# Kernel optimization log

Hardware: AMD Instinct MI355X
Metric: run time of the kernel (lower is better)

## Reference

```python
import jax, jax.numpy as jnp
import numpy as np
import math

EMBED_DIM = 1024
N_HEADS = 16
HEAD_DIM = EMBED_DIM // N_HEADS
B, N = 2, 2048


def setup_inputs() -> dict:
    key = jax.random.key(0)
    k1, k2, k3 = jax.random.split(key, 3)
    x = jax.random.normal(k1, (B, N, EMBED_DIM), dtype=jnp.float32)
    # Per-head Linear(D, 3*head_dim), stacked over heads. PyTorch Linear init scale ~1/sqrt(fan_in).
    bound = 1.0 / math.sqrt(EMBED_DIM)
    Wkqv = jax.random.uniform(k2, (N_HEADS, EMBED_DIM, 3 * HEAD_DIM), dtype=jnp.float32, minval=-bound, maxval=bound)
    bkqv = jax.random.uniform(k3, (N_HEADS, 3 * HEAD_DIM), dtype=jnp.float32, minval=-bound, maxval=bound)
    return {"x": x, "Wkqv": Wkqv, "bkqv": bkqv}


def reference(x, Wkqv, bkqv):
    Bx, Nx, D = x.shape
    hd = Wkqv.shape[-1] // 3
    # all heads at once: [B, H, N, 3*hd]
    proj = jnp.einsum('bnd,hdf->bhnf', x, Wkqv) + bkqv[None, :, None, :]
    # torch.split order in the original is (k, q, v)
    k, q, v = jnp.split(proj, 3, axis=-1)
    # scores = q @ k^T / sqrt(head_dim)   [B, H, N, N]
    scores = jnp.einsum('bhqd,bhkd->bhqk', q, k) / math.sqrt(hd)
    causal = jnp.tril(jnp.ones((Nx, Nx), dtype=bool))
    scores = jnp.where(causal[None, None, :, :], scores, -jnp.inf)
    attn = jax.nn.softmax(scores, axis=-1)
    out = jnp.einsum('bhqk,bhkd->bhqd', attn, v)  # [B, H, N, hd]
    # concat heads -> [B, N, D]  (forward() passes no out_matrix, so no output projection)
    return out.transpose(0, 2, 1, 3).reshape(Bx, Nx, D)
```

## Files before the change

### kernel.cpp

```cpp
#include <hip/hip_runtime.h>
#include <math.h>

typedef float f32x4 __attribute__((ext_vector_type(4)));
typedef __bf16 bf16x8 __attribute__((ext_vector_type(8)));
typedef __bf16 bf16x4 __attribute__((ext_vector_type(4)));

#define MFMA16(a, b, c) __builtin_amdgcn_mfma_f32_16x16x32_bf16((a), (b), (c), 0, 0, 0)

constexpr int Bsz = 2, Nseq = 2048, Dm = 1024, Hh = 16, HDim = 64, F3 = 192;
constexpr int Mrows = Bsz * Nseq;
constexpr int NC = Hh * F3;
constexpr float QSCALE = 0.125f * 1.4426950408889634f;

__device__ inline void load_lds16(const void* g, void* l) {
    __builtin_amdgcn_global_load_lds((const __attribute__((address_space(1))) void*)g,
                                     (__attribute__((address_space(3))) void*)l, 16, 0, 0);
}

#define FENCE asm volatile("" ::: "memory")
#define BARRIER do { FENCE; __builtin_amdgcn_s_barrier(); FENCE; } while (0)


__global__ __launch_bounds__(256) void conv_x_kernel(const float* __restrict__ x,
                                                     __bf16* __restrict__ xb) {
    int i = blockIdx.x * 256 + threadIdx.x;
    const float4* xv = reinterpret_cast<const float4*>(x);
    float4 a = xv[2 * i];
    float4 b = xv[2 * i + 1];
    bf16x8 o = {(__bf16)a.x, (__bf16)a.y, (__bf16)a.z, (__bf16)a.w,
                (__bf16)b.x, (__bf16)b.y, (__bf16)b.z, (__bf16)b.w};
    *reinterpret_cast<bf16x8*>(xb + 8 * i) = o;
}

__global__ __launch_bounds__(256) void conv_w_kernel(const float* __restrict__ w,
                                                     __bf16* __restrict__ wt) {
    __shared__ __bf16 tile[32][66];
    int h = blockIdx.z, d0 = blockIdx.x * 32, c0 = blockIdx.y * 64;
    for (int i = threadIdx.x; i < 32 * 64; i += 256) {
        int di = i >> 6, cj = i & 63;
        tile[di][cj] = (__bf16)w[(size_t)(h * Dm + d0 + di) * F3 + c0 + cj];
    }
    __syncthreads();
    for (int i = threadIdx.x; i < 32 * 64; i += 256) {
        int ci = i >> 5, dj = i & 31;
        wt[(size_t)(h * F3 + c0 + ci) * Dm + d0 + dj] = tile[dj][ci];
    }
}

__global__ __launch_bounds__(512, 2) void gemm_proj(const __bf16* __restrict__ xb,
                                                    const __bf16* __restrict__ wt,
                                                    const float* __restrict__ bias,
                                                    __bf16* __restrict__ kbuf,
                                                    __bf16* __restrict__ qbuf,
                                                    __bf16* __restrict__ vt) {
    __shared__ __align__(16) __bf16 Ab[2][256 * 64];
    __shared__ __align__(16) __bf16 Bb[2][192 * 64];

    int flat = blockIdx.x;
    int swz = (flat & 7) * 32 + (flat >> 3);
    int bm = swz >> 4, bn = swz & 15;
    int r0 = bm * 256, n0 = bn * 192;

    int w = threadIdx.x >> 6, lane = threadIdx.x & 63;
    int col = lane & 15, quad = lane >> 4;
    int wm = w >> 2, wn = w & 3;

    f32x4 acc[8][3] = {};

    int rl = lane >> 3;
    int cg = ((lane & 7) ^ rl) * 8;

    auto stage = [&](int t, int s) {
#pragma unroll
        for (int i = 0; i < 4; i++) {
            int rowb = w * 32 + i * 8;
            load_lds16(xb + (size_t)(r0 + rowb + rl) * Dm + t * 64 + cg,
                       &Ab[s][rowb * 64]);
        }
#pragma unroll
        for (int i = 0; i < 3; i++) {
            int rowb = w * 24 + i * 8;
            load_lds16(wt + (size_t)(n0 + rowb + rl) * Dm + t * 64 + cg,
                       &Bb[s][rowb * 64]);
        }
    };

    stage(0, 0);
    stage(1, 1);

    for (int j = 0; j < 16; j++) {
        int s = j & 1;
        if (j < 15) asm volatile("s_waitcnt vmcnt(7)" ::: "memory");
        else        asm volatile("s_waitcnt vmcnt(0)" ::: "memory");
        BARRIER;

#pragma unroll
        for (int ks = 0; ks < 2; ks++) {
            int cq = ks * 4 + quad;
            bf16x8 af[8], bfr[3];
#pragma unroll
            for (int mt = 0; mt < 8; mt++) {
                int row = wm * 128 + mt * 16 + col;
                af[mt] = *reinterpret_cast<const bf16x8*>(
                    &Ab[s][row * 64 + ((cq ^ (row & 7)) * 8)]);
            }
#pragma unroll
            for (int nt = 0; nt < 3; nt++) {
                int row = wn * 48 + nt * 16 + col;
                bfr[nt] = *reinterpret_cast<const bf16x8*>(
                    &Bb[s][row * 64 + ((cq ^ (row & 7)) * 8)]);
            }
            __builtin_amdgcn_s_setprio(1);
#pragma unroll
            for (int mt = 0; mt < 8; mt++)
#pragma unroll
                for (int nt = 0; nt < 3; nt++)
                    acc[mt][nt] = MFMA16(af[mt], bfr[nt], acc[mt][nt]);
            __builtin_amdgcn_s_setprio(0);
        }

        BARRIER;
        if (j + 2 < 16) stage(j + 2, s);
    }

#pragma unroll
    for (int nt = 0; nt < 3; nt++) {
        int g = n0 + wn * 48 + nt * 16 + col;
        int h = g / F3, c = g - h * F3;
        float bv = bias[g];
        bool isq = (c >= 64 && c < 128), isv = (c >= 128);
        int cd = c & 63;
#pragma unroll
        for (int mt = 0; mt < 8; mt++) {
#pragma unroll
            for (int rg = 0; rg < 4; rg++) {
                int r = r0 + wm * 128 + mt * 16 + quad * 4 + rg;
                int b = r >> 11, n = r & (Nseq - 1);
                float v = acc[mt][nt][rg] + bv;
                if (isq) v *= QSCALE;
                size_t bh = (size_t)(b * Hh + h);
                if (isv) {
                    int np = (n & ~63) | ((n & 15) << 2) | ((n >> 4) & 3);
                    vt[(bh * HDim + cd) * Nseq + np] = (__bf16)v;
                } else {
                    ((isq) ? qbuf : kbuf)[(bh * Nseq + n) * HDim + cd] = (__bf16)v;
                }
            }
        }
    }
}

__global__ __launch_bounds__(256) void proj_small(const float* __restrict__ x,
                                                  const __bf16* __restrict__ wt,
                                                  const float* __restrict__ bias,
                                                  __bf16* __restrict__ kbuf,
                                                  __bf16* __restrict__ qbuf,
                                                  __bf16* __restrict__ vt) {
    int h = blockIdx.y;
    int wave = threadIdx.x >> 6, lane = threadIdx.x & 63;
    int col = lane & 15, quad = lane >> 4;
    int r0 = blockIdx.x * 128 + wave * 32;

    f32x4 acc[12][2] = {};
    const float* xr0 = x + (size_t)(r0 + col) * Dm + quad * 8;
    const float* xr1 = xr0 + 16 * Dm;
    const __bf16* wbase = wt + (size_t)(h * F3 + col) * Dm + quad * 8;

    for (int k0 = 0; k0 < Dm; k0 += 32) {
        float4 a0lo = *reinterpret_cast<const float4*>(xr0 + k0);
        float4 a0hi = *reinterpret_cast<const float4*>(xr0 + k0 + 4);
        float4 a1lo = *reinterpret_cast<const float4*>(xr1 + k0);
        float4 a1hi = *reinterpret_cast<const float4*>(xr1 + k0 + 4);
        bf16x8 a0 = {(__bf16)a0lo.x, (__bf16)a0lo.y, (__bf16)a0lo.z, (__bf16)a0lo.w,
                     (__bf16)a0hi.x, (__bf16)a0hi.y, (__bf16)a0hi.z, (__bf16)a0hi.w};
        bf16x8 a1 = {(__bf16)a1lo.x, (__bf16)a1lo.y, (__bf16)a1lo.z, (__bf16)a1lo.w,
                     (__bf16)a1hi.x, (__bf16)a1hi.y, (__bf16)a1hi.z, (__bf16)a1hi.w};
#pragma unroll
        for (int ct = 0; ct < 12; ct++) {
            bf16x8 bf = *reinterpret_cast<const bf16x8*>(wbase + ct * 16 * Dm + k0);
            acc[ct][0] = MFMA16(a0, bf, acc[ct][0]);
            acc[ct][1] = MFMA16(a1, bf, acc[ct][1]);
        }
    }
#pragma unroll
    for (int ct = 0; ct < 12; ct++) {
        int c = ct * 16 + col;
        float bv = bias[h * F3 + c];
        int cd = c & 63;
        bool isq = (c >= 64 && c < 128), isv = (c >= 128);
#pragma unroll
        for (int rt = 0; rt < 2; rt++) {
#pragma unroll
            for (int rg = 0; rg < 4; rg++) {
                int r = r0 + rt * 16 + quad * 4 + rg;
                int b = r >> 11, n = r & (Nseq - 1);
                float v = acc[ct][rt][rg] + bv;
                if (isq) v *= QSCALE;
                size_t bh = (size_t)(b * Hh + h);
                if (isv) {
                    int np = (n & ~63) | ((n & 15) << 2) | ((n >> 4) & 3);
                    vt[(bh * HDim + cd) * Nseq + np] = (__bf16)v;
                } else {
                    ((isq) ? qbuf : kbuf)[(bh * Nseq + n) * HDim + cd] = (__bf16)v;
                }
            }
        }
    }
}

__global__ __launch_bounds__(256) void attn_kernel(const __bf16* __restrict__ qbuf,
                                                   const __bf16* __restrict__ kbuf,
                                                   const __bf16* __restrict__ vt,
                                                   float* __restrict__ out) {
    __shared__ __align__(16) __bf16 Kb[2][64 * 64];
    __shared__ __align__(16) __bf16 Vb[2][64 * 64];
    __shared__ __align__(16) __bf16 plds[4][16][72];
    int bh = blockIdx.x;
    int b = bh >> 4, h = bh & 15;
    int tile = 31 - blockIdx.y;
    int wave = threadIdx.x >> 6, lane = threadIdx.x & 63;
    int col = lane & 15, quad = lane >> 4;
    int q0 = tile * 64 + wave * 16;

    const __bf16* qbase = qbuf + (size_t)bh * Nseq * HDim;
    const __bf16* kbase = kbuf + (size_t)bh * Nseq * HDim;
    const __bf16* vbase = vt + (size_t)bh * HDim * Nseq;

    bf16x8 aq0 = *reinterpret_cast<const bf16x8*>(qbase + (q0 + col) * HDim + quad * 8);
    bf16x8 aq1 = *reinterpret_cast<const bf16x8*>(qbase + (q0 + col) * HDim + quad * 8 + 32);

    const bf16x8 vone = {(__bf16)1.f, (__bf16)1.f, (__bf16)1.f, (__bf16)1.f,
                         (__bf16)1.f, (__bf16)1.f, (__bf16)1.f, (__bf16)1.f};

    f32x4 o[4] = {};
    f32x4 ls = {};

    int mb = tile * 64;
    int loop_end = mb + 64;

    int rl = lane >> 3;
    int srow0 = wave * 16 + rl;
    int srow1 = wave * 16 + 8 + rl;
    int sc = (lane & 7) ^ rl;
    const __bf16* ksrc0 = kbase + srow0 * HDim + sc * 8;
    const __bf16* ksrc1 = kbase + srow1 * HDim + sc * 8;
    const __bf16* vsrc0 = vbase + (size_t)srow0 * Nseq + sc * 8;
    const __bf16* vsrc1 = vbase + (size_t)srow1 * Nseq + sc * 8;
    int d0 = wave * 1024, d1 = wave * 1024 + 512;

    int sw0 = ((quad ^ (col & 7)) * 8);
    int sw1 = (((quad + 4) ^ (col & 7)) * 8);

    load_lds16(ksrc0, &Kb[0][d0]);
    load_lds16(ksrc1, &Kb[0][d1]);
    load_lds16(vsrc0, &Vb[0][d0]);
    load_lds16(vsrc1, &Vb[0][d1]);
    FENCE;

    int s = 0;
    for (int kb = 0; kb < loop_end; kb += 64) {
        asm volatile("s_waitcnt vmcnt(0)" ::: "memory");
        BARRIER;
        int nkb = kb + 64;
        if (nkb < loop_end) {
            load_lds16(ksrc0 + nkb * HDim, &Kb[s ^ 1][d0]);
            load_lds16(ksrc1 + nkb * HDim, &Kb[s ^ 1][d1]);
            load_lds16(vsrc0 + nkb, &Vb[s ^ 1][d0]);
            load_lds16(vsrc1 + nkb, &Vb[s ^ 1][d1]);
        }

        bool masked = (kb == mb);
        const __bf16* Kcur = Kb[s];
        const __bf16* Vcur = Vb[s];
        f32x4 z = {};
        f32x4 sc4[4];
#pragma unroll
        for (int g = 0; g < 4; g++) {
            const __bf16* krow = Kcur + (col + 16 * g) * 64;
            bf16x8 k0 = *reinterpret_cast<const bf16x8*>(krow + sw0);
            bf16x8 k1 = *reinterpret_cast<const bf16x8*>(krow + sw1);
            sc4[g] = MFMA16(aq0, k0, z);
            sc4[g] = MFMA16(aq1, k1, sc4[g]);
        }
        if (masked) {
#pragma unroll
            for (int r = 0; r < 4; r++) {
                int qi = q0 + quad * 4 + r;
                bf16x4 pk;
#pragma unroll
                for (int g = 0; g < 4; g++) {
                    float p = (kb + col + 16 * g <= qi) ? exp2f(sc4[g][r]) : 0.f;
                    pk[g] = (__bf16)p;
                }
                *reinterpret_cast<bf16x4*>(&plds[wave][quad * 4 + r][col * 4]) = pk;
            }
        } else {
#pragma unroll
            for (int r = 0; r < 4; r++) {
                bf16x4 pk;
#pragma unroll
                for (int g = 0; g < 4; g++) pk[g] = (__bf16)exp2f(sc4[g][r]);
                *reinterpret_cast<bf16x4*>(&plds[wave][quad * 4 + r][col * 4]) = pk;
            }
        }
        bf16x8 pa0 = *reinterpret_cast<const bf16x8*>(&plds[wave][col][quad * 8]);
        bf16x8 pa1 = *reinterpret_cast<const bf16x8*>(&plds[wave][col][32 + quad * 8]);
        ls = MFMA16(pa0, vone, ls);
        ls = MFMA16(pa1, vone, ls);
#pragma unroll
        for (int nt = 0; nt < 4; nt++) {
            const __bf16* vrow = Vcur + (col + 16 * nt) * 64;
            bf16x8 v0 = *reinterpret_cast<const bf16x8*>(vrow + sw0);
            bf16x8 v1 = *reinterpret_cast<const bf16x8*>(vrow + sw1);
            o[nt] = MFMA16(pa0, v0, o[nt]);
            o[nt] = MFMA16(pa1, v1, o[nt]);
        }
        s ^= 1;
    }

    float linv[4];
#pragma unroll
    for (int r = 0; r < 4; r++) linv[r] = 1.f / ls[r];
#pragma unroll
    for (int nt = 0; nt < 4; nt++) {
#pragma unroll
        for (int r = 0; r < 4; r++) {
            int qi = q0 + quad * 4 + r;
            out[((size_t)(b * Nseq + qi)) * Dm + h * HDim + nt * 16 + col] = o[nt][r] * linv[r];
        }
    }
}

extern "C" void kernel_launch(void* const* d_in, const int* in_sizes, int n_in,
                              void* d_out, int out_size, void* d_ws, size_t ws_size,
                              hipStream_t stream) {
    const float* x = nullptr;
    const float* w = nullptr;
    const float* bias = nullptr;
    for (int i = 0; i < n_in; i++) {
        if (in_sizes[i] == Mrows * Dm) x = (const float*)d_in[i];
        else if (in_sizes[i] == Hh * Dm * F3) w = (const float*)d_in[i];
        else if (in_sizes[i] == Hh * F3) bias = (const float*)d_in[i];
    }
    float* outp = (float*)d_out;

    char* ws = (char*)d_ws;
    __bf16* wt = (__bf16*)(ws);
    __bf16* kbuf = (__bf16*)(ws + 6291456);
    __bf16* qbuf = (__bf16*)(ws + 6291456 + 8388608);
    __bf16* vt = (__bf16*)(ws + 6291456 + 2 * 8388608);
    __bf16* xb = (__bf16*)(ws + 6291456 + 3 * 8388608);

    conv_w_kernel<<<dim3(Dm / 32, F3 / 64, Hh), 256, 0, stream>>>(w, wt);
    if (ws_size >= (size_t)(6291456 + 4 * 8388608)) {
        conv_x_kernel<<<Mrows * Dm / (8 * 256), 256, 0, stream>>>(x, xb);
        gemm_proj<<<dim3((Mrows / 256) * (NC / 192)), 512, 0, stream>>>(xb, wt, bias, kbuf, qbuf, vt);
    } else {
        proj_small<<<dim3(Mrows / 128, Hh), 256, 0, stream>>>(x, wt, bias, kbuf, qbuf, vt);
    }
    attn_kernel<<<dim3(32, 32), 256, 0, stream>>>(qbuf, kbuf, vt, outp);
}
```

Before: 159.2 us.

## Fuse x/W conversion kernels, swizzle P LDS layout, drop prefetch guard

Merges the x-to-bf16 and weight transpose conversion kernels into a single launch that dispatches on block index, removing one kernel launch. In the attention kernel, the probability scratch buffer switches from a padded layout to an XOR-swizzled 64-wide layout to reduce LDS bank conflicts on the write and read. The prefetch branch is removed, so the last iteration issues an out-of-tile load into the unused buffer, which reads a little beyond the current tile.

New measurement: 155.8 us. 1.02x faster.

```diff
diff --git a/kernel.cpp b/kernel.cpp
--- a/kernel.cpp
+++ b/kernel.cpp
@@ -21,15 +21,33 @@
 #define BARRIER do { FENCE; __builtin_amdgcn_s_barrier(); FENCE; } while (0)
 
 
-__global__ __launch_bounds__(256) void conv_x_kernel(const float* __restrict__ x,
-                                                     __bf16* __restrict__ xb) {
-    int i = blockIdx.x * 256 + threadIdx.x;
-    const float4* xv = reinterpret_cast<const float4*>(x);
-    float4 a = xv[2 * i];
-    float4 b = xv[2 * i + 1];
-    bf16x8 o = {(__bf16)a.x, (__bf16)a.y, (__bf16)a.z, (__bf16)a.w,
-                (__bf16)b.x, (__bf16)b.y, (__bf16)b.z, (__bf16)b.w};
-    *reinterpret_cast<bf16x8*>(xb + 8 * i) = o;
+__global__ __launch_bounds__(256) void conv_xw_kernel(const float* __restrict__ x,
+                                                      __bf16* __restrict__ xb,
+                                                      const float* __restrict__ w,
+                                                      __bf16* __restrict__ wt) {
+    __shared__ __bf16 tile[32][66];
+    if (blockIdx.x < 2048) {
+        int i = blockIdx.x * 256 + threadIdx.x;
+        const float4* xv = reinterpret_cast<const float4*>(x);
+        float4 a = xv[2 * i];
+        float4 b = xv[2 * i + 1];
+        bf16x8 o = {(__bf16)a.x, (__bf16)a.y, (__bf16)a.z, (__bf16)a.w,
+                    (__bf16)b.x, (__bf16)b.y, (__bf16)b.z, (__bf16)b.w};
+        *reinterpret_cast<bf16x8*>(xb + 8 * i) = o;
+    } else {
+        int id = blockIdx.x - 2048;
+        int h = id / 96, rem = id % 96;
+        int d0 = (rem & 31) * 32, c0 = (rem >> 5) * 64;
+        for (int i = threadIdx.x; i < 32 * 64; i += 256) {
+            int di = i >> 6, cj = i & 63;
+            tile[di][cj] = (__bf16)w[(size_t)(h * Dm + d0 + di) * F3 + c0 + cj];
+        }
+        __syncthreads();
+        for (int i = threadIdx.x; i < 32 * 64; i += 256) {
+            int ci = i >> 5, dj = i & 31;
+            wt[(size_t)(h * F3 + c0 + ci) * Dm + d0 + dj] = tile[dj][ci];
+        }
+    }
 }
 
 __global__ __launch_bounds__(256) void conv_w_kernel(const float* __restrict__ w,
@@ -214,7 +232,7 @@
                                                    float* __restrict__ out) {
     __shared__ __align__(16) __bf16 Kb[2][64 * 64];
     __shared__ __align__(16) __bf16 Vb[2][64 * 64];
-    __shared__ __align__(16) __bf16 plds[4][16][72];
+    __shared__ __align__(16) __bf16 plds[4][16 * 64];
     int bh = blockIdx.x;
     int b = bh >> 4, h = bh & 15;
     int tile = 31 - blockIdx.y;
@@ -251,6 +269,9 @@
     int sw0 = ((quad ^ (col & 7)) * 8);
     int sw1 = (((quad + 4) ^ (col & 7)) * 8);
 
+    int pr0 = col * 64 + ((quad ^ (col & 7)) << 3);
+    int pr1 = col * 64 + (((quad + 4) ^ (col & 7)) << 3);
+
     load_lds16(ksrc0, &Kb[0][d0]);
     load_lds16(ksrc1, &Kb[0][d1]);
     load_lds16(vsrc0, &Vb[0][d0]);
@@ -262,12 +283,10 @@
         asm volatile("s_waitcnt vmcnt(0)" ::: "memory");
         BARRIER;
         int nkb = kb + 64;
-        if (nkb < loop_end) {
-            load_lds16(ksrc0 + nkb * HDim, &Kb[s ^ 1][d0]);
-            load_lds16(ksrc1 + nkb * HDim, &Kb[s ^ 1][d1]);
-            load_lds16(vsrc0 + nkb, &Vb[s ^ 1][d0]);
-            load_lds16(vsrc1 + nkb, &Vb[s ^ 1][d1]);
-        }
+        load_lds16(ksrc0 + nkb * HDim, &Kb[s ^ 1][d0]);
+        load_lds16(ksrc1 + nkb * HDim, &Kb[s ^ 1][d1]);
+        load_lds16(vsrc0 + nkb, &Vb[s ^ 1][d0]);
+        load_lds16(vsrc1 + nkb, &Vb[s ^ 1][d1]);
 
         bool masked = (kb == mb);
         const __bf16* Kcur = Kb[s];
@@ -285,26 +304,30 @@
         if (masked) {
 #pragma unroll
             for (int r = 0; r < 4; r++) {
-                int qi = q0 + quad * 4 + r;
+                int row = quad * 4 + r;
+                int qi = q0 + row;
                 bf16x4 pk;
 #pragma unroll
                 for (int g = 0; g < 4; g++) {
                     float p = (kb + col + 16 * g <= qi) ? exp2f(sc4[g][r]) : 0.f;
                     pk[g] = (__bf16)p;
                 }
-                *reinterpret_cast<bf16x4*>(&plds[wave][quad * 4 + r][col * 4]) = pk;
+                *reinterpret_cast<bf16x4*>(
+                    &plds[wave][row * 64 + ((col ^ ((row & 7) << 1)) << 2)]) = pk;
             }
         } else {
 #pragma unroll
             for (int r = 0; r < 4; r++) {
+                int row = quad * 4 + r;
                 bf16x4 pk;
 #pragma unroll
                 for (int g = 0; g < 4; g++) pk[g] = (__bf16)exp2f(sc4[g][r]);
-                *reinterpret_cast<bf16x4*>(&plds[wave][quad * 4 + r][col * 4]) = pk;
-            }
-        }
-        bf16x8 pa0 = *reinterpret_cast<const bf16x8*>(&plds[wave][col][quad * 8]);
-        bf16x8 pa1 = *reinterpret_cast<const bf16x8*>(&plds[wave][col][32 + quad * 8]);
+                *reinterpret_cast<bf16x4*>(
+                    &plds[wave][row * 64 + ((col ^ ((row & 7) << 1)) << 2)]) = pk;
+            }
+        }
+        bf16x8 pa0 = *reinterpret_cast<const bf16x8*>(&plds[wave][pr0]);
+        bf16x8 pa1 = *reinterpret_cast<const bf16x8*>(&plds[wave][pr1]);
         ls = MFMA16(pa0, vone, ls);
         ls = MFMA16(pa1, vone, ls);
 #pragma unroll
@@ -351,11 +374,11 @@
     __bf16* vt = (__bf16*)(ws + 6291456 + 2 * 8388608);
     __bf16* xb = (__bf16*)(ws + 6291456 + 3 * 8388608);
 
-    conv_w_kernel<<<dim3(Dm / 32, F3 / 64, Hh), 256, 0, stream>>>(w, wt);
     if (ws_size >= (size_t)(6291456 + 4 * 8388608)) {
-        conv_x_kernel<<<Mrows * Dm / (8 * 256), 256, 0, stream>>>(x, xb);
+        conv_xw_kernel<<<3584, 256, 0, stream>>>(x, xb, w, wt);
         gemm_proj<<<dim3((Mrows / 256) * (NC / 192)), 512, 0, stream>>>(xb, wt, bias, kbuf, qbuf, vt);
     } else {
+        conv_w_kernel<<<dim3(Dm / 32, F3 / 64, Hh), 256, 0, stream>>>(w, wt);
         proj_small<<<dim3(Mrows / 128, Hh), 256, 0, stream>>>(x, wt, bias, kbuf, qbuf, vt);
     }
     attn_kernel<<<dim3(32, 32), 256, 0, stream>>>(qbuf, kbuf, vt, outp);
```
